# Performance work log

Hardware: AMD Instinct MI355X
Metric: run time of the kernel (lower is better)

The kernel has to match this reference:

```python
import jax, jax.numpy as jnp
import numpy as np

EMBED_DIM = 1024
WINDOW = 256
NUM_HEADS = 16
HEAD_DIM = EMBED_DIM // NUM_HEADS
SCALE = HEAD_DIM ** (-0.5)


def setup_inputs() -> dict:
    key = jax.random.key(0)
    ks = jax.random.split(key, 9)
    B, S, E = 4, 4096, EMBED_DIM
    std = E ** (-0.5)
    x = jax.random.normal(ks[0], (B, S, E), dtype=jnp.float32)
    Wq = jax.random.normal(ks[1], (E, E), dtype=jnp.float32) * std
    Wk = jax.random.normal(ks[2], (E, E), dtype=jnp.float32) * std
    Wv = jax.random.normal(ks[3], (E, E), dtype=jnp.float32) * std
    Wo = jax.random.normal(ks[4], (E, E), dtype=jnp.float32) * std
    bq = jax.random.normal(ks[5], (E,), dtype=jnp.float32) * 0.01
    bk = jax.random.normal(ks[6], (E,), dtype=jnp.float32) * 0.01
    bv = jax.random.normal(ks[7], (E,), dtype=jnp.float32) * 0.01
    bo = jax.random.normal(ks[8], (E,), dtype=jnp.float32) * 0.01
    return {"x": x, "Wq": Wq, "bq": bq, "Wk": Wk, "bk": bk,
            "Wv": Wv, "bv": bv, "Wo": Wo, "bo": bo}


def reference(x, Wq, bq, Wk, bk, Wv, bv, Wo, bo):
    B, S, E = x.shape
    W = WINDOW
    nw = S // W  # seq_len chosen divisible by window_size
    # projections (torch Linear: x @ W.T + b); no head split in the original
    q = x @ Wq.T + bq
    k = x @ Wk.T + bk
    v = x @ Wv.T + bv
    # split into non-overlapping windows: [B, nw, W, E]
    qw = q.reshape(B, nw, W, E)
    kw = k.reshape(B, nw, W, E)
    vw = v.reshape(B, nw, W, E)
    scores = jnp.einsum('bnqe,bnke->bnqk', qw, kw) * SCALE  # [B, nw, W, W]
    causal = jnp.tril(jnp.ones((W, W), dtype=bool))
    scores = jnp.where(causal, scores, -jnp.inf)
    attn = jax.nn.softmax(scores, axis=-1)
    out = jnp.einsum('bnqk,bnke->bnqe', attn, vw).reshape(B, S, E)
    out = out @ Wo.T + bo
    return out + x
```

## Files before the change

### kernel.cpp

```cpp
#include <hip/hip_runtime.h>
#include <hip/hip_bf16.h>


typedef unsigned short u16;
typedef __attribute__((ext_vector_type(8))) short short8;
typedef __attribute__((ext_vector_type(4))) float f32x4;

__device__ __forceinline__ u16 f2bf(float f) {
    __hip_bfloat16 h = __float2bfloat16(f);
    return __builtin_bit_cast(u16, h);
}

__global__ void cast_x(const float* __restrict__ x, u16* __restrict__ xb, u16* __restrict__ xt) {
    __shared__ float lt[64][65];
    const int t = threadIdx.x;
    const int e0 = blockIdx.x * 64, i0 = blockIdx.y * 64;
    const int tr = t >> 3, tc = (t & 7) * 8;
#pragma unroll
    for (int p = 0; p < 2; ++p) {
        int r = p * 32 + tr;
        const float* s = x + (size_t)(i0 + r) * 1024 + e0 + tc;
        float4 a = *(const float4*)s, b = *(const float4*)(s + 4);
        short8 o;
        o[0] = (short)f2bf(a.x); o[1] = (short)f2bf(a.y); o[2] = (short)f2bf(a.z); o[3] = (short)f2bf(a.w);
        o[4] = (short)f2bf(b.x); o[5] = (short)f2bf(b.y); o[6] = (short)f2bf(b.z); o[7] = (short)f2bf(b.w);
        *(short8*)(xb + (size_t)(i0 + r) * 1024 + e0 + tc) = o;
        lt[r][tc + 0] = a.x; lt[r][tc + 1] = a.y; lt[r][tc + 2] = a.z; lt[r][tc + 3] = a.w;
        lt[r][tc + 4] = b.x; lt[r][tc + 5] = b.y; lt[r][tc + 6] = b.z; lt[r][tc + 7] = b.w;
    }
    __syncthreads();
#pragma unroll
    for (int p = 0; p < 2; ++p) {
        int r = p * 32 + tr;
        short8 o;
#pragma unroll
        for (int j = 0; j < 8; ++j) o[j] = (short)f2bf(lt[tc + j][r]);
        *(short8*)(xt + (size_t)(e0 + r) * 16384 + i0 + tc) = o;
    }
}

__global__ void wcast(const float* __restrict__ Wq, const float* __restrict__ Wk,
                      const float* __restrict__ Wv, const float* __restrict__ Wo,
                      u16* __restrict__ WqT, u16* __restrict__ WkT,
                      u16* __restrict__ WvT, u16* __restrict__ Wob)
{
    __shared__ float lt[64][65];
    const int which = blockIdx.x >> 8;
    const int bid = blockIdx.x & 255;
    const int c0 = (bid & 15) * 64, r0 = (bid >> 4) * 64;
    const int t = threadIdx.x;
    const int tr = t >> 3, tc = (t & 7) * 8;
    const float* src = which == 0 ? Wq : which == 1 ? Wk : which == 2 ? Wv : Wo;
    if (which == 3) {
#pragma unroll
        for (int p = 0; p < 2; ++p) {
            int r = p * 32 + tr;
            const float* s = src + (size_t)(r0 + r) * 1024 + c0 + tc;
            float4 a = *(const float4*)s, b = *(const float4*)(s + 4);
            short8 o;
            o[0] = (short)f2bf(a.x); o[1] = (short)f2bf(a.y); o[2] = (short)f2bf(a.z); o[3] = (short)f2bf(a.w);
            o[4] = (short)f2bf(b.x); o[5] = (short)f2bf(b.y); o[6] = (short)f2bf(b.z); o[7] = (short)f2bf(b.w);
            *(short8*)(Wob + (size_t)(r0 + r) * 1024 + c0 + tc) = o;
        }
        return;
    }
    u16* dst = which == 0 ? WqT : which == 1 ? WkT : WvT;
#pragma unroll
    for (int p = 0; p < 2; ++p) {
        int r = p * 32 + tr;
        const float* s = src + (size_t)(r0 + r) * 1024 + c0 + tc;
        float4 a = *(const float4*)s, b = *(const float4*)(s + 4);
        lt[r][tc + 0] = a.x; lt[r][tc + 1] = a.y; lt[r][tc + 2] = a.z; lt[r][tc + 3] = a.w;
        lt[r][tc + 4] = b.x; lt[r][tc + 5] = b.y; lt[r][tc + 6] = b.z; lt[r][tc + 7] = b.w;
    }
    __syncthreads();
#pragma unroll
    for (int p = 0; p < 2; ++p) {
        int r = p * 32 + tr;
        short8 o;
#pragma unroll
        for (int j = 0; j < 8; ++j) o[j] = (short)f2bf(lt[tc + j][r]);
        *(short8*)(dst + (size_t)(c0 + r) * 1024 + r0 + tc) = o;
    }
}

__global__ void ub2(const float* __restrict__ Wk, const float* __restrict__ bq,
                    const float* __restrict__ Wo, const float* __restrict__ bv,
                    const float* __restrict__ bo, float* __restrict__ u, float* __restrict__ b2)
{
    const int t = threadIdx.x, bid = blockIdx.x;
    if (bid < 4) {
        int b = bid * 256 + t;
        float acc = 0.f;
        for (int o = 0; o < 1024; ++o) acc += Wk[(size_t)o * 1024 + b] * bq[o];
        u[b] = acc;
    } else {
        int n = (bid - 4) * 16 + (t >> 4);
        int l = t & 15;
        float acc = 0.f;
        for (int m = l; m < 1024; m += 16) acc += Wo[(size_t)n * 1024 + m] * bv[m];
#pragma unroll
        for (int s = 1; s < 16; s <<= 1) acc += __shfl_xor(acc, s, 64);
        if (l == 0) b2[n] = acc + bo[n];
    }
}

__global__ __launch_bounds__(256, 4) void gemm_small_dual(
    const u16* __restrict__ HA, const u16* __restrict__ HB, u16* __restrict__ HC,
    const u16* __restrict__ WA, const u16* __restrict__ WB, u16* __restrict__ WC)
{
    __shared__ __align__(16) u16 At[64 * 64], Bt[64 * 64];
    const bool sec = blockIdx.x >= 256;
    const u16* A = sec ? WA : HA;
    const u16* B = sec ? WB : HB;
    u16* C = sec ? WC : HC;
    const int bid = blockIdx.x & 255;
    const int m0 = (bid >> 4) * 64, n0 = (bid & 15) * 64;
    const int t = threadIdx.x, lane = t & 63, w = t >> 6;
    const int l15 = lane & 15, lk = lane >> 4;

    f32x4 acc[4];
#pragma unroll
    for (int m = 0; m < 4; ++m) acc[m] = (f32x4){0.f, 0.f, 0.f, 0.f};

    for (int k0 = 0; k0 < 1024; k0 += 64) {
        __syncthreads();
#pragma unroll
        for (int p = 0; p < 2; ++p) {
            int e = p * 2048 + t * 8;
            int row = e >> 6, col = e & 63;
            short8 va = *(const short8*)(A + (size_t)(m0 + row) * 1024 + k0 + col);
            *(short8*)((char*)At + row * 128 + ((col * 2) ^ ((row & 7) << 4))) = va;
            short8 vb = *(const short8*)(B + (size_t)(n0 + row) * 1024 + k0 + col);
            *(short8*)((char*)Bt + row * 128 + ((col * 2) ^ ((row & 7) << 4))) = vb;
        }
        __syncthreads();
#pragma unroll
        for (int ks = 0; ks < 2; ++ks) {
            int bc = ks * 64 + lk * 16;
            int brow = w * 16 + l15;
            short8 bfr = *(const short8*)((char*)Bt + brow * 128 + (bc ^ ((brow & 7) << 4)));
#pragma unroll
            for (int m = 0; m < 4; ++m) {
                int arow = m * 16 + l15;
                short8 af = *(const short8*)((char*)At + arow * 128 + (bc ^ ((arow & 7) << 4)));
                acc[m] = __builtin_amdgcn_mfma_f32_16x16x32_bf16(af, bfr, acc[m], 0, 0, 0);
            }
        }
    }
#pragma unroll
    for (int m = 0; m < 4; ++m)
#pragma unroll
        for (int r = 0; r < 4; ++r) {
            int row = m0 + m * 16 + lk * 4 + r;
            int col = n0 + w * 16 + l15;
            C[(size_t)row * 1024 + col] = f2bf(acc[m][r]);
        }
}

template <int EPI>
__global__ __launch_bounds__(512, 4) void gemm_bt(
    const u16* __restrict__ A, const u16* __restrict__ B,
    int M, int N, int K,
    const float* __restrict__ bias0,
    u16* __restrict__ Cb, float* __restrict__ Cf, const float* __restrict__ resid)
{
    __shared__ __align__(16) u16 At[128 * 64];
    __shared__ __align__(16) u16 Bt[128 * 64];
    const int t = threadIdx.x;
    const int lane = t & 63;
    const int w = t >> 6;
    const int wm = w >> 2, wn = w & 3;
    const int l15 = lane & 15, lk = lane >> 4;

    const int bid = blockIdx.y * gridDim.x + blockIdx.x;
    const int nwg = gridDim.x * gridDim.y;
    const int cpx = nwg >> 3;
    const int swz = (bid & 7) * cpx + (bid >> 3);
    const int tn = swz & 7;
    const int tm = swz >> 3;
    const int m0 = tm * 128, n0 = tn * 128;

    const int srow = t >> 3, scol = (t & 7) * 8;

    f32x4 acc[4][2];
#pragma unroll
    for (int mf = 0; mf < 4; ++mf)
#pragma unroll
        for (int nf = 0; nf < 2; ++nf)
            acc[mf][nf] = (f32x4){0.f, 0.f, 0.f, 0.f};

    for (int k0 = 0; k0 < K; k0 += 64) {
        __syncthreads();
#pragma unroll
        for (int p = 0; p < 2; ++p) {
            int row = p * 64 + srow;
            short8 va = *(const short8*)(A + (size_t)(m0 + row) * K + k0 + scol);
            *(short8*)((char*)At + row * 128 + ((scol * 2) ^ ((row & 7) << 4))) = va;
            short8 vb = *(const short8*)(B + (size_t)(n0 + row) * K + k0 + scol);
            *(short8*)((char*)Bt + row * 128 + ((scol * 2) ^ ((row & 7) << 4))) = vb;
        }
        __syncthreads();
#pragma unroll
        for (int ks = 0; ks < 2; ++ks) {
            const int bc = ks * 64 + lk * 16;
            short8 af[4], bfr[2];
#pragma unroll
            for (int mf = 0; mf < 4; ++mf) {
                int row = wm * 64 + mf * 16 + l15;
                af[mf] = *(const short8*)((char*)At + row * 128 + (bc ^ ((row & 7) << 4)));
            }
#pragma unroll
            for (int nf = 0; nf < 2; ++nf) {
                int row = wn * 32 + nf * 16 + l15;
                bfr[nf] = *(const short8*)((char*)Bt + row * 128 + (bc ^ ((row & 7) << 4)));
            }
#pragma unroll
            for (int mf = 0; mf < 4; ++mf)
#pragma unroll
                for (int nf = 0; nf < 2; ++nf)
                    acc[mf][nf] = __builtin_amdgcn_mfma_f32_16x16x32_bf16(af[mf], bfr[nf], acc[mf][nf], 0, 0, 0);
        }
    }

#pragma unroll
    for (int mf = 0; mf < 4; ++mf) {
#pragma unroll
        for (int nf = 0; nf < 2; ++nf) {
            int col = n0 + wn * 32 + nf * 16 + l15;
            float bv = bias0[col];
#pragma unroll
            for (int r = 0; r < 4; ++r) {
                int row = m0 + wm * 64 + mf * 16 + lk * 4 + r;
                float v = acc[mf][nf][r] + bv;
                if (EPI == 0)
                    Cb[(size_t)row * N + col] = f2bf(v);
                else
                    Cf[(size_t)row * N + col] = v + resid[(size_t)row * N + col];
            }
        }
    }
}

__global__ __launch_bounds__(256, 2) void attn_win(
    const u16* __restrict__ y, const u16* __restrict__ xb,
    const u16* __restrict__ xt, u16* __restrict__ z)
{
    __shared__ __align__(16) char smem[54272];
    u16* Qt = (u16*)smem;
    u16* Kt = (u16*)(smem + 4096);
    u16* Vl = (u16*)smem;
    u16* P  = (u16*)(smem + 36864);
    float* rmax = (float*)(smem + 53248);
    float* rsum = (float*)(smem + 53760);

    const int t = threadIdx.x;
    const int lane = t & 63, wv = t >> 6;
    const int l15 = lane & 15, lk = lane >> 4;
    const int bid = blockIdx.x;
    const int swz = (bid & 7) * 64 + (bid >> 3);
    const int win = swz >> 3, qc = swz & 7;
    const size_t qrow0 = (size_t)win * 256 + qc * 32;
    const size_t krow0 = (size_t)win * 256;

    f32x4 acc[2][4];
#pragma unroll
    for (int m = 0; m < 2; ++m)
#pragma unroll
        for (int n = 0; n < 4; ++n)
            acc[m][n] = (f32x4){0.f, 0.f, 0.f, 0.f};

    for (int e0 = 0; e0 < 1024; e0 += 64) {
        __syncthreads();
        {
            int row = t >> 3, col = (t & 7) * 8;
            short8 v = *(const short8*)(y + (qrow0 + row) * 1024 + e0 + col);
            *(short8*)((char*)Qt + row * 128 + ((col * 2) ^ ((row & 7) << 4))) = v;
        }
#pragma unroll
        for (int p = 0; p < 8; ++p) {
            int e = p * 2048 + t * 8;
            int row = e >> 6, col = e & 63;
            short8 v = *(const short8*)(xb + (krow0 + row) * 1024 + e0 + col);
            *(short8*)((char*)Kt + row * 128 + ((col * 2) ^ ((row & 7) << 4))) = v;
        }
        __syncthreads();
#pragma unroll
        for (int ks = 0; ks < 2; ++ks) {
            const int bc = ks * 64 + lk * 16;
            short8 af[2], bfr[4];
#pragma unroll
            for (int m = 0; m < 2; ++m) {
                int row = m * 16 + l15;
                af[m] = *(const short8*)((char*)Qt + row * 128 + (bc ^ ((row & 7) << 4)));
            }
#pragma unroll
            for (int n = 0; n < 4; ++n) {
                int row = wv * 64 + n * 16 + l15;
                bfr[n] = *(const short8*)((char*)Kt + row * 128 + (bc ^ ((row & 7) << 4)));
            }
            __builtin_amdgcn_s_setprio(1);
#pragma unroll
            for (int m = 0; m < 2; ++m)
#pragma unroll
                for (int n = 0; n < 4; ++n)
                    acc[m][n] = __builtin_amdgcn_mfma_f32_16x16x32_bf16(af[m], bfr[n], acc[m][n], 0, 0, 0);
            __builtin_amdgcn_s_setprio(0);
        }
    }

#pragma unroll
    for (int m = 0; m < 2; ++m)
#pragma unroll
        for (int n = 0; n < 4; ++n) {
            int col = wv * 64 + n * 16 + l15;
#pragma unroll
            for (int r = 0; r < 4; ++r) {
                int qpos = qc * 32 + m * 16 + lk * 4 + r;
                float v = acc[m][n][r] * 0.125f;
                acc[m][n][r] = (col <= qpos) ? v : -1e30f;
            }
        }
#pragma unroll
    for (int m = 0; m < 2; ++m)
#pragma unroll
        for (int r = 0; r < 4; ++r) {
            float tmx = fmaxf(fmaxf(acc[m][0][r], acc[m][1][r]), fmaxf(acc[m][2][r], acc[m][3][r]));
            tmx = fmaxf(tmx, __shfl_xor(tmx, 1));
            tmx = fmaxf(tmx, __shfl_xor(tmx, 2));
            tmx = fmaxf(tmx, __shfl_xor(tmx, 4));
            tmx = fmaxf(tmx, __shfl_xor(tmx, 8));
            if (l15 == 0) rmax[(m * 16 + lk * 4 + r) * 4 + wv] = tmx;
        }
    __syncthreads();
#pragma unroll
    for (int m = 0; m < 2; ++m)
#pragma unroll
        for (int r = 0; r < 4; ++r) {
            int row = m * 16 + lk * 4 + r;
            float m4 = fmaxf(fmaxf(rmax[row * 4], rmax[row * 4 + 1]),
                             fmaxf(rmax[row * 4 + 2], rmax[row * 4 + 3]));
            float s = 0.f;
#pragma unroll
            for (int n = 0; n < 4; ++n) {
                float e = __expf(acc[m][n][r] - m4);
                acc[m][n][r] = e;
                s += e;
            }
            s += __shfl_xor(s, 1);
            s += __shfl_xor(s, 2);
            s += __shfl_xor(s, 4);
            s += __shfl_xor(s, 8);
            if (l15 == 0) rsum[row * 4 + wv] = s;
        }
    __syncthreads();
#pragma unroll
    for (int m = 0; m < 2; ++m)
#pragma unroll
        for (int r = 0; r < 4; ++r) {
            int row = m * 16 + lk * 4 + r;
            float inv = 1.f / (rsum[row * 4] + rsum[row * 4 + 1] + rsum[row * 4 + 2] + rsum[row * 4 + 3]);
#pragma unroll
            for (int n = 0; n < 4; ++n) {
                int col = wv * 64 + n * 16 + l15;
                *(u16*)((char*)P + row * 512 + ((col * 2) ^ ((row & 7) << 4))) = f2bf(acc[m][n][r] * inv);
            }
        }

    for (int n0 = 0; n0 < 1024; n0 += 64) {
        __syncthreads();
#pragma unroll
        for (int p = 0; p < 8; ++p) {
            int e = p * 2048 + t * 8;
            int row = e >> 8, col = e & 255;
            short8 v = *(const short8*)(xt + (size_t)(n0 + row) * 16384 + win * 256 + col);
            *(short8*)((char*)Vl + row * 512 + ((col * 2) ^ ((row & 7) << 4))) = v;
        }
        __syncthreads();
        f32x4 acc2[2];
#pragma unroll
        for (int m = 0; m < 2; ++m) acc2[m] = (f32x4){0.f, 0.f, 0.f, 0.f};
#pragma unroll
        for (int ks = 0; ks < 8; ++ks) {
            const int bc = ks * 64 + lk * 16;
            short8 af[2];
#pragma unroll
            for (int m = 0; m < 2; ++m) {
                int row = m * 16 + l15;
                af[m] = *(const short8*)((char*)P + row * 512 + (bc ^ ((row & 7) << 4)));
            }
            int vrow = wv * 16 + l15;
            short8 bfr = *(const short8*)((char*)Vl + vrow * 512 + (bc ^ ((vrow & 7) << 4)));
            __builtin_amdgcn_s_setprio(1);
#pragma unroll
            for (int m = 0; m < 2; ++m)
                acc2[m] = __builtin_amdgcn_mfma_f32_16x16x32_bf16(af[m], bfr, acc2[m], 0, 0, 0);
            __builtin_amdgcn_s_setprio(0);
        }
#pragma unroll
        for (int m = 0; m < 2; ++m) {
#pragma unroll
            for (int r = 0; r < 4; ++r) {
                int row = m * 16 + lk * 4 + r;
                int col = n0 + wv * 16 + l15;
                z[(qrow0 + row) * 1024 + col] = f2bf(acc2[m][r]);
            }
        }
    }
}

extern "C" void kernel_launch(void* const* d_in, const int* in_sizes, int n_in,
                              void* d_out, int out_size, void* d_ws, size_t ws_size,
                              hipStream_t stream) {
    const float* x  = (const float*)d_in[0];
    const float* Wq = (const float*)d_in[1];
    const float* bq = (const float*)d_in[2];
    const float* Wk = (const float*)d_in[3];
    const float* Wv = (const float*)d_in[5];
    const float* bv = (const float*)d_in[6];
    const float* Wo = (const float*)d_in[7];
    const float* bo = (const float*)d_in[8];
    float* out = (float*)d_out;

    char* ws = (char*)d_ws;
    u16* xb  = (u16*)(ws);
    u16* xt  = (u16*)(ws + 33554432);
    u16* yb  = (u16*)(ws + 67108864);
    u16* zb  = (u16*)(ws + 100663296);
    u16* WqT = (u16*)(ws + 134217728);
    u16* WkT = (u16*)(ws + 136314880);
    u16* WvT = (u16*)(ws + 138412032);
    u16* Wob = (u16*)(ws + 140509184);
    u16* Hb  = (u16*)(ws + 142606336);
    u16* W2b = (u16*)(ws + 144703488);
    float* u_  = (float*)(ws + 146800640);
    float* b2_ = (float*)(ws + 146804736);

    cast_x<<<dim3(16, 256), 256, 0, stream>>>(x, xb, xt);
    wcast<<<1024, 256, 0, stream>>>(Wq, Wk, Wv, Wo, WqT, WkT, WvT, Wob);
    ub2<<<68, 256, 0, stream>>>(Wk, bq, Wo, bv, bo, u_, b2_);
    gemm_small_dual<<<512, 256, 0, stream>>>(WkT, WqT, Hb, Wob, WvT, W2b);
    gemm_bt<0><<<dim3(8, 128), 512, 0, stream>>>(xb, Hb, 16384, 1024, 1024, u_, yb, nullptr, nullptr);
    attn_win<<<512, 256, 0, stream>>>(yb, xb, xt, zb);
    gemm_bt<1><<<dim3(8, 128), 512, 0, stream>>>(zb, W2b, 16384, 1024, 1024, b2_, nullptr, out, x);
}
```

Baseline: 226.0 us.

## Fold output projection into value path and fuse epilogue into attention kernel

Uses associativity to apply the combined Wv·Wo weight (W2b) to x before attention, producing a transposed projected-V buffer in the same GEMM launch as the Y projection. The attention kernel then writes the fp32 output directly, adding the bias and the residual, which removes the final 16384x1024x1024 GEMM and the z intermediate. The x cast no longer writes a transposed copy. In exchange the first GEMM does twice the N work, and the attention epilogue now writes fp32 with extra residual reads.

```diff
diff --git a/kernel.cpp b/kernel.cpp
--- a/kernel.cpp
+++ b/kernel.cpp
@@ -4,6 +4,7 @@
 
 typedef unsigned short u16;
 typedef __attribute__((ext_vector_type(8))) short short8;
+typedef __attribute__((ext_vector_type(4))) short short4v;
 typedef __attribute__((ext_vector_type(4))) float f32x4;
 
 __device__ __forceinline__ u16 f2bf(float f) {
@@ -11,32 +12,15 @@
     return __builtin_bit_cast(u16, h);
 }
 
-__global__ void cast_x(const float* __restrict__ x, u16* __restrict__ xb, u16* __restrict__ xt) {
-    __shared__ float lt[64][65];
-    const int t = threadIdx.x;
-    const int e0 = blockIdx.x * 64, i0 = blockIdx.y * 64;
-    const int tr = t >> 3, tc = (t & 7) * 8;
-#pragma unroll
-    for (int p = 0; p < 2; ++p) {
-        int r = p * 32 + tr;
-        const float* s = x + (size_t)(i0 + r) * 1024 + e0 + tc;
-        float4 a = *(const float4*)s, b = *(const float4*)(s + 4);
-        short8 o;
-        o[0] = (short)f2bf(a.x); o[1] = (short)f2bf(a.y); o[2] = (short)f2bf(a.z); o[3] = (short)f2bf(a.w);
-        o[4] = (short)f2bf(b.x); o[5] = (short)f2bf(b.y); o[6] = (short)f2bf(b.z); o[7] = (short)f2bf(b.w);
-        *(short8*)(xb + (size_t)(i0 + r) * 1024 + e0 + tc) = o;
-        lt[r][tc + 0] = a.x; lt[r][tc + 1] = a.y; lt[r][tc + 2] = a.z; lt[r][tc + 3] = a.w;
-        lt[r][tc + 4] = b.x; lt[r][tc + 5] = b.y; lt[r][tc + 6] = b.z; lt[r][tc + 7] = b.w;
-    }
-    __syncthreads();
-#pragma unroll
-    for (int p = 0; p < 2; ++p) {
-        int r = p * 32 + tr;
-        short8 o;
-#pragma unroll
-        for (int j = 0; j < 8; ++j) o[j] = (short)f2bf(lt[tc + j][r]);
-        *(short8*)(xt + (size_t)(e0 + r) * 16384 + i0 + tc) = o;
-    }
+__global__ void cast_f32_bf16(const float* __restrict__ src, u16* __restrict__ dst, int n) {
+    int i = (blockIdx.x * 256 + threadIdx.x) * 8;
+    if (i >= n) return;
+    const float4* s = (const float4*)(src + i);
+    float4 a = s[0], b = s[1];
+    short8 o;
+    o[0] = (short)f2bf(a.x); o[1] = (short)f2bf(a.y); o[2] = (short)f2bf(a.z); o[3] = (short)f2bf(a.w);
+    o[4] = (short)f2bf(b.x); o[5] = (short)f2bf(b.y); o[6] = (short)f2bf(b.z); o[7] = (short)f2bf(b.w);
+    *(short8*)(dst + i) = o;
 }
 
 __global__ void wcast(const float* __restrict__ Wq, const float* __restrict__ Wk,
@@ -158,93 +142,102 @@
         }
 }
 
-template <int EPI>
-__global__ __launch_bounds__(512, 4) void gemm_bt(
-    const u16* __restrict__ A, const u16* __restrict__ B,
-    int M, int N, int K,
-    const float* __restrict__ bias0,
-    u16* __restrict__ Cb, float* __restrict__ Cf, const float* __restrict__ resid)
+__global__ __launch_bounds__(256, 2) void gemm_yv(
+    const u16* __restrict__ A, const u16* __restrict__ BH, const u16* __restrict__ BW,
+    const float* __restrict__ ub, u16* __restrict__ Y, u16* __restrict__ V2t)
 {
     __shared__ __align__(16) u16 At[128 * 64];
     __shared__ __align__(16) u16 Bt[128 * 64];
     const int t = threadIdx.x;
     const int lane = t & 63;
-    const int w = t >> 6;
-    const int wm = w >> 2, wn = w & 3;
+    const int wid = t >> 6;
+    const int wm = wid >> 1, wn = wid & 1;
     const int l15 = lane & 15, lk = lane >> 4;
+    const int K = 1024;
 
     const int bid = blockIdx.y * gridDim.x + blockIdx.x;
-    const int nwg = gridDim.x * gridDim.y;
-    const int cpx = nwg >> 3;
+    const int cpx = 2048 >> 3;
     const int swz = (bid & 7) * cpx + (bid >> 3);
-    const int tn = swz & 7;
-    const int tm = swz >> 3;
-    const int m0 = tm * 128, n0 = tn * 128;
-
-    const int srow = t >> 3, scol = (t & 7) * 8;
-
-    f32x4 acc[4][2];
-#pragma unroll
-    for (int mf = 0; mf < 4; ++mf)
-#pragma unroll
-        for (int nf = 0; nf < 2; ++nf)
-            acc[mf][nf] = (f32x4){0.f, 0.f, 0.f, 0.f};
+    const int tn = swz & 15;
+    const int tm = swz >> 4;
+    const int m0 = tm * 128;
+    const bool isv = tn >= 8;
+    const int n0 = (tn & 7) * 128;
+    const u16* B = isv ? BW : BH;
+
+    f32x4 acc[4][4];
+#pragma unroll
+    for (int m = 0; m < 4; ++m)
+#pragma unroll
+        for (int n = 0; n < 4; ++n)
+            acc[m][n] = (f32x4){0.f, 0.f, 0.f, 0.f};
 
     for (int k0 = 0; k0 < K; k0 += 64) {
         __syncthreads();
 #pragma unroll
-        for (int p = 0; p < 2; ++p) {
-            int row = p * 64 + srow;
-            short8 va = *(const short8*)(A + (size_t)(m0 + row) * K + k0 + scol);
-            *(short8*)((char*)At + row * 128 + ((scol * 2) ^ ((row & 7) << 4))) = va;
-            short8 vb = *(const short8*)(B + (size_t)(n0 + row) * K + k0 + scol);
-            *(short8*)((char*)Bt + row * 128 + ((scol * 2) ^ ((row & 7) << 4))) = vb;
+        for (int p = 0; p < 4; ++p) {
+            int e = p * 2048 + t * 8;
+            int row = e >> 6, col = e & 63;
+            short8 va = *(const short8*)(A + (size_t)(m0 + row) * K + k0 + col);
+            *(short8*)((char*)At + row * 128 + ((col * 2) ^ ((row & 7) << 4))) = va;
+            short8 vb = *(const short8*)(B + (size_t)(n0 + row) * K + k0 + col);
+            *(short8*)((char*)Bt + row * 128 + ((col * 2) ^ ((row & 7) << 4))) = vb;
         }
         __syncthreads();
 #pragma unroll
         for (int ks = 0; ks < 2; ++ks) {
             const int bc = ks * 64 + lk * 16;
-            short8 af[4], bfr[2];
-#pragma unroll
-            for (int mf = 0; mf < 4; ++mf) {
-                int row = wm * 64 + mf * 16 + l15;
-                af[mf] = *(const short8*)((char*)At + row * 128 + (bc ^ ((row & 7) << 4)));
-            }
-#pragma unroll
-            for (int nf = 0; nf < 2; ++nf) {
-                int row = wn * 32 + nf * 16 + l15;
-                bfr[nf] = *(const short8*)((char*)Bt + row * 128 + (bc ^ ((row & 7) << 4)));
-            }
-#pragma unroll
-            for (int mf = 0; mf < 4; ++mf)
-#pragma unroll
-                for (int nf = 0; nf < 2; ++nf)
-                    acc[mf][nf] = __builtin_amdgcn_mfma_f32_16x16x32_bf16(af[mf], bfr[nf], acc[mf][nf], 0, 0, 0);
-        }
-    }
-
-#pragma unroll
-    for (int mf = 0; mf < 4; ++mf) {
-#pragma unroll
-        for (int nf = 0; nf < 2; ++nf) {
-            int col = n0 + wn * 32 + nf * 16 + l15;
-            float bv = bias0[col];
-#pragma unroll
-            for (int r = 0; r < 4; ++r) {
-                int row = m0 + wm * 64 + mf * 16 + lk * 4 + r;
-                float v = acc[mf][nf][r] + bv;
-                if (EPI == 0)
-                    Cb[(size_t)row * N + col] = f2bf(v);
-                else
-                    Cf[(size_t)row * N + col] = v + resid[(size_t)row * N + col];
-            }
-        }
+            short8 af[4], bfr[4];
+#pragma unroll
+            for (int m = 0; m < 4; ++m) {
+                int row = wm * 64 + m * 16 + l15;
+                af[m] = *(const short8*)((char*)At + row * 128 + (bc ^ ((row & 7) << 4)));
+            }
+#pragma unroll
+            for (int n = 0; n < 4; ++n) {
+                int row = wn * 64 + n * 16 + l15;
+                bfr[n] = *(const short8*)((char*)Bt + row * 128 + (bc ^ ((row & 7) << 4)));
+            }
+#pragma unroll
+            for (int m = 0; m < 4; ++m)
+#pragma unroll
+                for (int n = 0; n < 4; ++n)
+                    acc[m][n] = __builtin_amdgcn_mfma_f32_16x16x32_bf16(af[m], bfr[n], acc[m][n], 0, 0, 0);
+        }
+    }
+
+    if (!isv) {
+#pragma unroll
+        for (int m = 0; m < 4; ++m)
+#pragma unroll
+            for (int n = 0; n < 4; ++n) {
+                int col = n0 + wn * 64 + n * 16 + l15;
+                float bv = ub[col];
+#pragma unroll
+                for (int r = 0; r < 4; ++r) {
+                    int row = m0 + wm * 64 + m * 16 + lk * 4 + r;
+                    Y[(size_t)row * 1024 + col] = f2bf(acc[m][n][r] + bv);
+                }
+            }
+    } else {
+#pragma unroll
+        for (int m = 0; m < 4; ++m)
+#pragma unroll
+            for (int n = 0; n < 4; ++n) {
+                int col = n0 + wn * 64 + n * 16 + l15;
+                int row0 = m0 + wm * 64 + m * 16 + lk * 4;
+                short4v pk;
+#pragma unroll
+                for (int r = 0; r < 4; ++r) pk[r] = (short)f2bf(acc[m][n][r]);
+                *(short4v*)(V2t + (size_t)col * 16384 + row0) = pk;
+            }
     }
 }
 
 __global__ __launch_bounds__(256, 2) void attn_win(
     const u16* __restrict__ y, const u16* __restrict__ xb,
-    const u16* __restrict__ xt, u16* __restrict__ z)
+    const u16* __restrict__ vt, const float* __restrict__ xres,
+    const float* __restrict__ b2, float* __restrict__ outp)
 {
     __shared__ __align__(16) char smem[54272];
     u16* Qt = (u16*)smem;
@@ -373,7 +366,7 @@
         for (int p = 0; p < 8; ++p) {
             int e = p * 2048 + t * 8;
             int row = e >> 8, col = e & 255;
-            short8 v = *(const short8*)(xt + (size_t)(n0 + row) * 16384 + win * 256 + col);
+            short8 v = *(const short8*)(vt + (size_t)(n0 + row) * 16384 + win * 256 + col);
             *(short8*)((char*)Vl + row * 512 + ((col * 2) ^ ((row & 7) << 4))) = v;
         }
         __syncthreads();
@@ -403,7 +396,8 @@
             for (int r = 0; r < 4; ++r) {
                 int row = m * 16 + lk * 4 + r;
                 int col = n0 + wv * 16 + l15;
-                z[(qrow0 + row) * 1024 + col] = f2bf(acc2[m][r]);
+                size_t idx = (qrow0 + row) * 1024 + col;
+                outp[idx] = acc2[m][r] + b2[col] + xres[idx];
             }
         }
     }
@@ -424,23 +418,21 @@
 
     char* ws = (char*)d_ws;
     u16* xb  = (u16*)(ws);
-    u16* xt  = (u16*)(ws + 33554432);
-    u16* yb  = (u16*)(ws + 67108864);
-    u16* zb  = (u16*)(ws + 100663296);
-    u16* WqT = (u16*)(ws + 134217728);
-    u16* WkT = (u16*)(ws + 136314880);
-    u16* WvT = (u16*)(ws + 138412032);
-    u16* Wob = (u16*)(ws + 140509184);
-    u16* Hb  = (u16*)(ws + 142606336);
-    u16* W2b = (u16*)(ws + 144703488);
-    float* u_  = (float*)(ws + 146800640);
-    float* b2_ = (float*)(ws + 146804736);
-
-    cast_x<<<dim3(16, 256), 256, 0, stream>>>(x, xb, xt);
+    u16* yb  = (u16*)(ws + 33554432);
+    u16* v2t = (u16*)(ws + 67108864);
+    u16* WqT = (u16*)(ws + 100663296);
+    u16* WkT = (u16*)(ws + 102760448);
+    u16* WvT = (u16*)(ws + 104857600);
+    u16* Wob = (u16*)(ws + 106954752);
+    u16* Hb  = (u16*)(ws + 109051904);
+    u16* W2b = (u16*)(ws + 111149056);
+    float* u_  = (float*)(ws + 113246208);
+    float* b2_ = (float*)(ws + 113250304);
+
+    cast_f32_bf16<<<8192, 256, 0, stream>>>(x, xb, 16777216);
     wcast<<<1024, 256, 0, stream>>>(Wq, Wk, Wv, Wo, WqT, WkT, WvT, Wob);
     ub2<<<68, 256, 0, stream>>>(Wk, bq, Wo, bv, bo, u_, b2_);
     gemm_small_dual<<<512, 256, 0, stream>>>(WkT, WqT, Hb, Wob, WvT, W2b);
-    gemm_bt<0><<<dim3(8, 128), 512, 0, stream>>>(xb, Hb, 16384, 1024, 1024, u_, yb, nullptr, nullptr);
-    attn_win<<<512, 256, 0, stream>>>(yb, xb, xt, zb);
-    gemm_bt<1><<<dim3(8, 128), 512, 0, stream>>>(zb, W2b, 16384, 1024, 1024, b2_, nullptr, out, x);
-}
+    gemm_yv<<<dim3(16, 128), 256, 0, stream>>>(xb, Hb, W2b, u_, yb, v2t);
+    attn_win<<<512, 256, 0, stream>>>(yb, xb, v2t, x, b2_, out);
+}
```

New measurement: 212.6 us. 5.9% less time.
